# Performance work log

Hardware: AMD Instinct MI355X
Metric: run time of the kernel (lower is better)

## Reference

```python
import jax, jax.numpy as jnp
import numpy as np

B, T, D, H = 4, 2048, 1024, 16
HD = D // H  # 64
NEG = -np.finfo(np.float32).max


def setup_inputs() -> dict:
    key = jax.random.key(0)
    ks = jax.random.split(key, 9)
    s = 1.0 / np.sqrt(D)
    return {
        "x": jax.random.normal(ks[0], (B, T, D), jnp.float32),
        "wq": jax.random.normal(ks[1], (D, D), jnp.float32) * s,
        "bq": jax.random.normal(ks[2], (D,), jnp.float32) * 0.02,
        "wk": jax.random.normal(ks[3], (D, D), jnp.float32) * s,
        "bk": jax.random.normal(ks[4], (D,), jnp.float32) * 0.02,
        "wv": jax.random.normal(ks[5], (D, D), jnp.float32) * s,
        "bv": jax.random.normal(ks[6], (D,), jnp.float32) * 0.02,
        "wo": jax.random.normal(ks[7], (D, D), jnp.float32) * s,
        "bo": jax.random.normal(ks[8], (D,), jnp.float32) * 0.02,
    }


def reference(x, wq, bq, wk, bk, wv, bv, wo, bo):
    b, t, d = x.shape
    # separate Q, K, V projections, reshape to (B, H, T, HD)
    def proj(w, bias):
        y = x @ w + bias
        return y.reshape(b, t, H, HD).transpose(0, 2, 1, 3)
    q = proj(wq, bq)
    k = proj(wk, bk)
    v = proj(wv, bv)
    scale = 1.0 / np.sqrt(HD).astype(np.float32)
    scores = jnp.einsum("bhqd,bhkd->bhqk", q, k) * scale  # (B,H,T,T)
    # causal mask: -max_float on strictly upper triangle (matches source)
    mask = jnp.triu(jnp.full((t, t), NEG, jnp.float32), k=1)
    attn = jax.nn.softmax(scores + mask, axis=-1)
    out = jnp.einsum("bhqk,bhkd->bhqd", attn, v)
    out = out.transpose(0, 2, 1, 3).reshape(b, t, d)
    return out @ wo + bo
```

## Files before the change

kernel.cpp:

```cpp
#include <hip/hip_runtime.h>

typedef __bf16 bf16x8 __attribute__((ext_vector_type(8)));
typedef float f32x4 __attribute__((ext_vector_type(4)));

#define B_ 4
#define T_ 2048
#define D_ 1024
#define H_ 16
#define HD_ 64
#define M_ 8192
#define QSCALE 0.1803368801111204f

__device__ __forceinline__ ushort f2b(float f) {
  union { float f; unsigned u; } v; v.f = f;
  unsigned u = v.u;
  return (ushort)((u + 0x7FFFu + ((u >> 16) & 1u)) >> 16);
}

__device__ __forceinline__ unsigned pkbf(float a, float b) {
  union { float f; unsigned u; } va, vb; va.f = a; vb.f = b;
  return __builtin_amdgcn_perm(vb.u + 0x8000u, va.u + 0x8000u, 0x07060302u);
}

__device__ __forceinline__ void gll16(const void* g, void* l) {
  __builtin_amdgcn_global_load_lds(
      (const __attribute__((address_space(1))) unsigned*)g,
      (__attribute__((address_space(3))) unsigned*)l, 16, 0, 0);
}

__global__ __launch_bounds__(256) void cast_x_kernel(const float* __restrict__ x,
                                                     ushort* __restrict__ xb) {
  int idx = blockIdx.x * 256 + threadIdx.x;
  float4 v = ((const float4*)x)[idx];
  ushort4 o;
  o.x = f2b(v.x); o.y = f2b(v.y); o.z = f2b(v.z); o.w = f2b(v.w);
  ((ushort4*)xb)[idx] = o;
}

__global__ __launch_bounds__(256) void transpose_w_kernel(
    const float* __restrict__ wq, const float* __restrict__ wk,
    const float* __restrict__ wv, const float* __restrict__ wo,
    ushort* __restrict__ wt_qkv, ushort* __restrict__ wt_o) {
  __shared__ float tile[32][33];
  int z = blockIdx.z;
  const float* src = (z == 0) ? wq : (z == 1) ? wk : (z == 2) ? wv : wo;
  ushort* dst = (z < 3) ? (wt_qkv + (size_t)z * D_ * D_) : wt_o;
  int n0 = blockIdx.x * 32, k0 = blockIdx.y * 32;
  int tx = threadIdx.x & 31, ty = threadIdx.x >> 5;
  for (int i = 0; i < 4; i++) {
    int r = ty + i * 8;
    tile[r][tx] = src[(size_t)(k0 + r) * D_ + n0 + tx];
  }
  __syncthreads();
  for (int i = 0; i < 4; i++) {
    int r = ty + i * 8;
    dst[(size_t)(n0 + r) * D_ + k0 + tx] = f2b(tile[tx][r]);
  }
}

__global__ __launch_bounds__(256) void gemm_kernel(
    const ushort* __restrict__ A, const ushort* __restrict__ Bt, int mode,
    const float* __restrict__ bias_q, const float* __restrict__ bias_k,
    const float* __restrict__ bias_v,
    ushort* __restrict__ qb, ushort* __restrict__ kb, ushort* __restrict__ vtb,
    float* __restrict__ outf) {
  __shared__ ushort As[2][128][64];
  __shared__ ushort Bs[2][128][64];
  int tid = threadIdx.x;
  int wave = tid >> 6, lane = tid & 63, lrow = lane >> 4, lcol = lane & 15;

  int gx = gridDim.x;
  int nwg = gx * gridDim.y;
  int orig = blockIdx.x + gx * blockIdx.y;
  int work = (orig & 7) * (nwg >> 3) + (orig >> 3);
  int m0 = (work / gx) * 128, n0 = (work % gx) * 128;
  int wm = (wave & 1) * 64, wn = (wave >> 1) * 64;

  int rb = tid >> 3;
  int dc = tid & 7;
  int scv = dc ^ (rb & 7);
  const ushort* aBase = A + (size_t)(m0 + rb) * D_ + scv * 8;
  const ushort* bBase = Bt + (size_t)(n0 + rb) * D_ + scv * 8;

  f32x4 zero = {0.f, 0.f, 0.f, 0.f};
  f32x4 acc[4][4];
  for (int i = 0; i < 4; i++)
    for (int j = 0; j < 4; j++) acc[i][j] = zero;

  int swz = lcol & 7;

  auto stage = [&](int buf, int k) {
#pragma unroll
    for (int g = 0; g < 4; g++) {
      gll16(aBase + (size_t)(32 * g) * D_ + k, &As[buf][0][0] + tid * 8 + g * 2048);
      gll16(bBase + (size_t)(32 * g) * D_ + k, &Bs[buf][0][0] + tid * 8 + g * 2048);
    }
  };

  stage(0, 0);

  for (int k0 = 0; k0 < D_; k0 += 64) {
    int cur = (k0 >> 6) & 1, nxt = cur ^ 1;
    __syncthreads();
    if (k0 + 64 < D_) stage(nxt, k0 + 64);

    for (int ks = 0; ks < 2; ks++) {
      bf16x8 af[4], bf[4];
      int ch = ((ks * 4 + lrow) ^ swz) * 8;
      for (int mt = 0; mt < 4; mt++)
        af[mt] = *(const bf16x8*)&As[cur][wm + mt * 16 + lcol][ch];
      for (int nt = 0; nt < 4; nt++)
        bf[nt] = *(const bf16x8*)&Bs[cur][wn + nt * 16 + lcol][ch];
      for (int mt = 0; mt < 4; mt++)
        for (int nt = 0; nt < 4; nt++)
          acc[mt][nt] = __builtin_amdgcn_mfma_f32_16x16x32_bf16(
              af[mt], bf[nt], acc[mt][nt], 0, 0, 0);
    }
  }

  if (mode == 0) {
    int proj = n0 >> 10;
    const float* bias = (proj == 0) ? bias_q : (proj == 1) ? bias_k : bias_v;
    for (int mt = 0; mt < 4; mt++) {
      int gm0 = m0 + wm + mt * 16 + lrow * 4;
      int b = gm0 >> 11, tp = gm0 & 2047;
      for (int nt = 0; nt < 4; nt++) {
        int gn = n0 + wn + nt * 16 + lcol;
        int inner = gn & 1023;
        int h = inner >> 6, hd = inner & 63;
        float bv = bias[inner];
        if (proj == 0) {
          size_t base = ((size_t)(b * H_ + h) * T_ + tp) * HD_ + hd;
          for (int r = 0; r < 4; r++)
            qb[base + (size_t)r * HD_] = f2b((acc[mt][nt][r] + bv) * QSCALE);
        } else if (proj == 1) {
          size_t base = ((size_t)(b * H_ + h) * T_ + tp) * HD_ + hd;
          for (int r = 0; r < 4; r++)
            kb[base + (size_t)r * HD_] = f2b(acc[mt][nt][r] + bv);
        } else {
          ushort4 pk;
          pk.x = f2b(acc[mt][nt][0] + bv);
          pk.y = f2b(acc[mt][nt][1] + bv);
          pk.z = f2b(acc[mt][nt][2] + bv);
          pk.w = f2b(acc[mt][nt][3] + bv);
          *(ushort4*)&vtb[((size_t)(b * H_ + h) * HD_ + hd) * T_ + tp] = pk;
        }
      }
    }
  } else {
    for (int mt = 0; mt < 4; mt++) {
      int gm0 = m0 + wm + mt * 16 + lrow * 4;
      for (int nt = 0; nt < 4; nt++) {
        int gn = n0 + wn + nt * 16 + lcol;
        float bv = bias_q[gn];
        for (int r = 0; r < 4; r++)
          outf[(size_t)(gm0 + r) * D_ + gn] = acc[mt][nt][r] + bv;
      }
    }
  }
}

__global__ __launch_bounds__(256) void flash_kernel(
    const ushort* __restrict__ qb, const ushort* __restrict__ kb,
    const ushort* __restrict__ vtb, ushort* __restrict__ ob) {
  __shared__ ushort Ks2[2][64][64];
  __shared__ ushort Vs2[2][64][64];
  __shared__ ushort Ps[4][32][64];
  int tid = threadIdx.x;
  int wave = tid >> 6, lane = tid & 63, lrow = lane >> 4, lcol = lane & 15;

  int bid = blockIdx.x + (blockIdx.y << 3);
  int xcd = bid & 7;
  int slot = bid >> 3;
  int bh = xcd * 8 + (slot >> 3);
  int p = slot & 7;
  int qb0 = 15 - p, qb1 = p;
  int b = bh >> 4, h = bh & 15;
  const ushort* qp = qb + (size_t)bh * T_ * HD_;
  const ushort* kh = kb + (size_t)bh * T_ * HD_;
  const ushort* vh = vtb + (size_t)bh * HD_ * T_;

  int n0 = 2 * qb0 + 2;
  int ntot = n0 + 2 * qb1 + 2;

  int r0 = tid >> 3, dc = tid & 7;
  int wsl = (dc ^ (r0 & 7)) * 8;
  int rsw = lcol & 7;

  uint4 kr0, kr1, vr0, vr1;
  auto gload = [&](int jt) {
    kr0 = *(const uint4*)&kh[(size_t)(jt * 64 + r0) * HD_ + dc * 8];
    kr1 = *(const uint4*)&kh[(size_t)(jt * 64 + r0 + 32) * HD_ + dc * 8];
    vr0 = *(const uint4*)&vh[(size_t)r0 * T_ + jt * 64 + dc * 8];
    vr1 = *(const uint4*)&vh[(size_t)(r0 + 32) * T_ + jt * 64 + dc * 8];
  };
  auto swrite = [&](int buf) {
    *(uint4*)&Ks2[buf][r0][wsl] = kr0;
    *(uint4*)&Ks2[buf][r0 + 32][wsl] = kr1;
    *(uint4*)&Vs2[buf][r0][wsl] = vr0;
    *(uint4*)&Vs2[buf][r0 + 32][wsl] = vr1;
  };

  bf16x8 af1;
  {
    __bf16 ov = (__bf16)((lcol == 0) ? 1.0f : 0.0f);
    for (int i2 = 0; i2 < 8; i2++) af1[i2] = ov;
  }

  f32x4 zero = {0.f, 0.f, 0.f, 0.f};

  gload(0);
  swrite(0);
  gload(1);
  __syncthreads();

  int q0wA = qb0 * 128 + wave * 32, q0wB = qb1 * 128 + wave * 32;
  bf16x8 qfA[2][2], qfB[2][2];
#pragma unroll
  for (int qh = 0; qh < 2; qh++)
#pragma unroll
    for (int ks = 0; ks < 2; ks++) {
      qfA[qh][ks] = *(const bf16x8*)&qp[(size_t)(q0wA + qh * 16 + lcol) * HD_ +
                                        ks * 32 + lrow * 8];
      qfB[qh][ks] = *(const bf16x8*)&qp[(size_t)(q0wB + qh * 16 + lcol) * HD_ +
                                        ks * 32 + lrow * 8];
    }

  auto run_pass = [&](int qblk, int q0w, int base, const bf16x8 qf[2][2]) {
    f32x4 accO[2][4];
    f32x4 accS[2];
#pragma unroll
    for (int qh = 0; qh < 2; qh++) {
      accS[qh] = zero;
      for (int mt = 0; mt < 4; mt++) accO[qh][mt] = zero;
    }

    int nj = 2 * qblk + 2;
    for (int j = 0; j < nj; j++) {
      int g = base + j, cur = g & 1;
      bool active = (j * 64 <= q0w + 31);

      if (active) {
        f32x4 st[2][4];
#pragma unroll
        for (int qh = 0; qh < 2; qh++)
          for (int mt = 0; mt < 4; mt++) st[qh][mt] = zero;
        __builtin_amdgcn_s_setprio(1);
#pragma unroll
        for (int ks = 0; ks < 2; ks++)
#pragma unroll
          for (int mt = 0; mt < 4; mt++) {
            bf16x8 kf = *(const bf16x8*)&Ks2[cur][mt * 16 + lcol]
                                            [((ks * 4 + lrow) ^ rsw) * 8];
            st[0][mt] = __builtin_amdgcn_mfma_f32_16x16x32_bf16(kf, qf[0][ks], st[0][mt], 0, 0, 0);
            st[1][mt] = __builtin_amdgcn_mfma_f32_16x16x32_bf16(kf, qf[1][ks], st[1][mt], 0, 0, 0);
          }
        __builtin_amdgcn_s_setprio(0);

        if (j >= 2 * qblk) {
#pragma unroll
          for (int qh = 0; qh < 2; qh++) {
            int q_g = q0w + qh * 16 + lcol;
#pragma unroll
            for (int mt = 0; mt < 4; mt++)
              for (int r = 0; r < 4; r++) {
                int kv_g = j * 64 + mt * 16 + lrow * 4 + r;
                if (kv_g > q_g) st[qh][mt][r] = -1e30f;
              }
          }
        }

#pragma unroll
        for (int qh = 0; qh < 2; qh++)
          for (int mt = 0; mt < 4; mt++)
            for (int r = 0; r < 4; r++)
              st[qh][mt][r] = __builtin_amdgcn_exp2f(st[qh][mt][r]);

#pragma unroll
        for (int qh = 0; qh < 2; qh++)
          for (int mt = 0; mt < 4; mt++) {
            uint2 pk;
            pk.x = pkbf(st[qh][mt][0], st[qh][mt][1]);
            pk.y = pkbf(st[qh][mt][2], st[qh][mt][3]);
            int sl = ((2 * mt + (lrow >> 1)) ^ rsw) * 8 + (lrow & 1) * 4;
            *(uint2*)&Ps[wave][qh * 16 + lcol][sl] = pk;
          }

        __builtin_amdgcn_s_setprio(1);
#pragma unroll
        for (int ks = 0; ks < 2; ks++) {
          int ch = ((ks * 4 + lrow) ^ rsw) * 8;
          bf16x8 pf0 = *(const bf16x8*)&Ps[wave][lcol][ch];
          bf16x8 pf1 = *(const bf16x8*)&Ps[wave][16 + lcol][ch];
          accS[0] = __builtin_amdgcn_mfma_f32_16x16x32_bf16(af1, pf0, accS[0], 0, 0, 0);
          accS[1] = __builtin_amdgcn_mfma_f32_16x16x32_bf16(af1, pf1, accS[1], 0, 0, 0);
#pragma unroll
          for (int mt = 0; mt < 4; mt++) {
            bf16x8 vf = *(const bf16x8*)&Vs2[cur][mt * 16 + lcol][ch];
            accO[0][mt] = __builtin_amdgcn_mfma_f32_16x16x32_bf16(vf, pf0, accO[0][mt], 0, 0, 0);
            accO[1][mt] = __builtin_amdgcn_mfma_f32_16x16x32_bf16(vf, pf1, accO[1][mt], 0, 0, 0);
          }
        }
        __builtin_amdgcn_s_setprio(0);
      }

      if (g + 1 < ntot) swrite(cur ^ 1);
      if (g + 2 < ntot) {
        int s = g + 2;
        gload(s < n0 ? s : s - n0);
      }
      __syncthreads();
    }

#pragma unroll
    for (int qh = 0; qh < 2; qh++) {
      float lsum = __shfl(accS[qh][0], lcol);
      float linv = 1.f / lsum;
      int t = q0w + qh * 16 + lcol;
      size_t base2 = ((size_t)b * T_ + t) * D_ + h * HD_;
#pragma unroll
      for (int mt = 0; mt < 4; mt++) {
        uint2 pk;
        pk.x = pkbf(accO[qh][mt][0] * linv, accO[qh][mt][1] * linv);
        pk.y = pkbf(accO[qh][mt][2] * linv, accO[qh][mt][3] * linv);
        *(uint2*)&ob[base2 + mt * 16 + lrow * 4] = pk;
      }
    }
  };

  run_pass(qb0, q0wA, 0, qfA);
  run_pass(qb1, q0wB, n0, qfB);
}

extern "C" void kernel_launch(void* const* d_in, const int* in_sizes, int n_in,
                              void* d_out, int out_size, void* d_ws, size_t ws_size,
                              hipStream_t stream) {
  (void)in_sizes; (void)n_in; (void)out_size; (void)ws_size;
  const float* x  = (const float*)d_in[0];
  const float* wq = (const float*)d_in[1];
  const float* bq = (const float*)d_in[2];
  const float* wk = (const float*)d_in[3];
  const float* bk = (const float*)d_in[4];
  const float* wv = (const float*)d_in[5];
  const float* bv = (const float*)d_in[6];
  const float* wo = (const float*)d_in[7];
  const float* bo = (const float*)d_in[8];
  float* out = (float*)d_out;

  char* ws = (char*)d_ws;
  ushort* xb     = (ushort*)(ws);
  ushort* wt_qkv = (ushort*)(ws + 16777216);
  ushort* wt_o   = (ushort*)(ws + 23068672);
  ushort* qb     = (ushort*)(ws + 25165824);
  ushort* kb     = (ushort*)(ws + 41943040);
  ushort* vtb    = (ushort*)(ws + 58720256);
  ushort* ob     = (ushort*)(ws + 75497472);

  cast_x_kernel<<<8192, 256, 0, stream>>>(x, xb);
  transpose_w_kernel<<<dim3(32, 32, 4), 256, 0, stream>>>(wq, wk, wv, wo, wt_qkv, wt_o);
  gemm_kernel<<<dim3(24, 64), 256, 0, stream>>>(xb, wt_qkv, 0, bq, bk, bv, qb, kb, vtb, nullptr);
  flash_kernel<<<dim3(8, 64), 256, 0, stream>>>(qb, kb, vtb, ob);
  gemm_kernel<<<dim3(8, 64), 256, 0, stream>>>(ob, wt_o, 1, bo, nullptr, nullptr,
                                               nullptr, nullptr, nullptr, out);
}
```

Before: 247.0 us.

## Share K/V tiles between paired query blocks and vectorize Q/K epilogue stores

The flash kernel now processes both paired query blocks (15-p and p) in one loop over key/value tiles. Each K/V tile staged in LDS feeds both blocks, instead of the kernel making two sequential passes that reload the smaller block's tiles. This needs two sets of output accumulators in registers, which may raise register pressure and lower occupancy. It also remaps block-to-head assignment with a phase that alternates pairing order. Separately, the Q/K projection epilogue uses lane shuffles and byte permutes to assemble four contiguous bf16 values per lane, replacing scattered 2-byte stores with 8-byte stores.

```diff
diff --git a/kernel.cpp b/kernel.cpp
--- a/kernel.cpp
+++ b/kernel.cpp
@@ -121,23 +121,46 @@
   if (mode == 0) {
     int proj = n0 >> 10;
     const float* bias = (proj == 0) ? bias_q : (proj == 1) ? bias_k : bias_v;
-    for (int mt = 0; mt < 4; mt++) {
-      int gm0 = m0 + wm + mt * 16 + lrow * 4;
-      int b = gm0 >> 11, tp = gm0 & 2047;
-      for (int nt = 0; nt < 4; nt++) {
-        int gn = n0 + wn + nt * 16 + lcol;
-        int inner = gn & 1023;
-        int h = inner >> 6, hd = inner & 63;
-        float bv = bias[inner];
-        if (proj == 0) {
-          size_t base = ((size_t)(b * H_ + h) * T_ + tp) * HD_ + hd;
-          for (int r = 0; r < 4; r++)
-            qb[base + (size_t)r * HD_] = f2b((acc[mt][nt][r] + bv) * QSCALE);
-        } else if (proj == 1) {
-          size_t base = ((size_t)(b * H_ + h) * T_ + tp) * HD_ + hd;
-          for (int r = 0; r < 4; r++)
-            kb[base + (size_t)r * HD_] = f2b(acc[mt][nt][r] + bv);
-        } else {
+    if (proj < 2) {
+      ushort* dst = (proj == 0) ? qb : kb;
+      bool isq = (proj == 0);
+      int c0 = lcol & 1, c1 = lcol & 2;
+      for (int mt = 0; mt < 4; mt++) {
+        int gm0 = m0 + wm + mt * 16 + lrow * 4;
+        int t = gm0 + (lcol & 3);
+        int b = t >> 11, tp = t & 2047;
+        for (int nt = 0; nt < 4; nt++) {
+          int gn = n0 + wn + nt * 16 + lcol;
+          int inner = gn & 1023;
+          float bv = bias[inner];
+          float v0 = acc[mt][nt][0] + bv, v1 = acc[mt][nt][1] + bv;
+          float v2 = acc[mt][nt][2] + bv, v3 = acc[mt][nt][3] + bv;
+          if (isq) { v0 *= QSCALE; v1 *= QSCALE; v2 *= QSCALE; v3 *= QSCALE; }
+          unsigned p0 = ((unsigned)f2b(v1) << 16) | f2b(v0);
+          unsigned p1 = ((unsigned)f2b(v3) << 16) | f2b(v2);
+          unsigned x0 = __shfl_xor(p0, 1), x1 = __shfl_xor(p1, 1);
+          unsigned a0 = c0 ? __builtin_amdgcn_perm(p0, x0, 0x07060302u)
+                           : __builtin_amdgcn_perm(x0, p0, 0x05040100u);
+          unsigned a1 = c0 ? __builtin_amdgcn_perm(p1, x1, 0x07060302u)
+                           : __builtin_amdgcn_perm(x1, p1, 0x05040100u);
+          unsigned y0 = __shfl_xor(a0, 2), y1 = __shfl_xor(a1, 2);
+          uint2 q2;
+          q2.x = c1 ? y1 : a0;
+          q2.y = c1 ? a1 : y0;
+          int innerb = (n0 + wn + nt * 16 + (lcol & ~3)) & 1023;
+          int h = innerb >> 6, hd0 = innerb & 63;
+          *(uint2*)&dst[((size_t)(b * H_ + h) * T_ + tp) * HD_ + hd0] = q2;
+        }
+      }
+    } else {
+      for (int mt = 0; mt < 4; mt++) {
+        int gm0 = m0 + wm + mt * 16 + lrow * 4;
+        int b = gm0 >> 11, tp = gm0 & 2047;
+        for (int nt = 0; nt < 4; nt++) {
+          int gn = n0 + wn + nt * 16 + lcol;
+          int inner = gn & 1023;
+          int h = inner >> 6, hd = inner & 63;
+          float bv = bias[inner];
           ushort4 pk;
           pk.x = f2b(acc[mt][nt][0] + bv);
           pk.y = f2b(acc[mt][nt][1] + bv);
@@ -160,6 +183,72 @@
   }
 }
 
+#define QCOMP(qblk_, q0w_, qfv, accOv, accSv)                                   \
+  do {                                                                          \
+    f32x4 st[2][4];                                                             \
+    for (int qh = 0; qh < 2; qh++)                                              \
+      for (int mt = 0; mt < 4; mt++) st[qh][mt] = zero;                         \
+    __builtin_amdgcn_s_setprio(1);                                              \
+    _Pragma("unroll")                                                           \
+    for (int ks = 0; ks < 2; ks++)                                              \
+      _Pragma("unroll")                                                         \
+      for (int mt = 0; mt < 4; mt++) {                                          \
+        bf16x8 kf = *(const bf16x8*)&Ks2[cur][mt * 16 + lcol]                   \
+                                        [((ks * 4 + lrow) ^ rsw) * 8];          \
+        st[0][mt] = __builtin_amdgcn_mfma_f32_16x16x32_bf16(kf, qfv[0][ks],     \
+                                                            st[0][mt], 0, 0, 0);\
+        st[1][mt] = __builtin_amdgcn_mfma_f32_16x16x32_bf16(kf, qfv[1][ks],     \
+                                                            st[1][mt], 0, 0, 0);\
+      }                                                                         \
+    __builtin_amdgcn_s_setprio(0);                                              \
+    if (j >= 2 * (qblk_)) {                                                     \
+      _Pragma("unroll")                                                         \
+      for (int qh = 0; qh < 2; qh++) {                                          \
+        int q_g = (q0w_) + qh * 16 + lcol;                                      \
+        _Pragma("unroll")                                                       \
+        for (int mt = 0; mt < 4; mt++)                                          \
+          for (int r = 0; r < 4; r++) {                                         \
+            int kv_g = j * 64 + mt * 16 + lrow * 4 + r;                         \
+            if (kv_g > q_g) st[qh][mt][r] = -1e30f;                             \
+          }                                                                     \
+      }                                                                         \
+    }                                                                           \
+    _Pragma("unroll")                                                           \
+    for (int qh = 0; qh < 2; qh++)                                              \
+      for (int mt = 0; mt < 4; mt++)                                            \
+        for (int r = 0; r < 4; r++)                                             \
+          st[qh][mt][r] = __builtin_amdgcn_exp2f(st[qh][mt][r]);                \
+    _Pragma("unroll")                                                           \
+    for (int qh = 0; qh < 2; qh++)                                              \
+      for (int mt = 0; mt < 4; mt++) {                                          \
+        uint2 pk;                                                               \
+        pk.x = pkbf(st[qh][mt][0], st[qh][mt][1]);                              \
+        pk.y = pkbf(st[qh][mt][2], st[qh][mt][3]);                              \
+        int sl = ((2 * mt + (lrow >> 1)) ^ rsw) * 8 + (lrow & 1) * 4;           \
+        *(uint2*)&Ps[wave][qh * 16 + lcol][sl] = pk;                            \
+      }                                                                         \
+    __builtin_amdgcn_s_setprio(1);                                              \
+    _Pragma("unroll")                                                           \
+    for (int ks = 0; ks < 2; ks++) {                                            \
+      int ch = ((ks * 4 + lrow) ^ rsw) * 8;                                     \
+      bf16x8 pf0 = *(const bf16x8*)&Ps[wave][lcol][ch];                         \
+      bf16x8 pf1 = *(const bf16x8*)&Ps[wave][16 + lcol][ch];                    \
+      accSv[0] = __builtin_amdgcn_mfma_f32_16x16x32_bf16(af1, pf0, accSv[0],    \
+                                                         0, 0, 0);              \
+      accSv[1] = __builtin_amdgcn_mfma_f32_16x16x32_bf16(af1, pf1, accSv[1],    \
+                                                         0, 0, 0);              \
+      _Pragma("unroll")                                                         \
+      for (int mt = 0; mt < 4; mt++) {                                          \
+        bf16x8 vf = *(const bf16x8*)&Vs2[cur][mt * 16 + lcol][ch];              \
+        accOv[0][mt] = __builtin_amdgcn_mfma_f32_16x16x32_bf16(vf, pf0,         \
+                                                    accOv[0][mt], 0, 0, 0);     \
+        accOv[1][mt] = __builtin_amdgcn_mfma_f32_16x16x32_bf16(vf, pf1,         \
+                                                    accOv[1][mt], 0, 0, 0);     \
+      }                                                                         \
+    }                                                                           \
+    __builtin_amdgcn_s_setprio(0);                                              \
+  } while (0)
+
 __global__ __launch_bounds__(256) void flash_kernel(
     const ushort* __restrict__ qb, const ushort* __restrict__ kb,
     const ushort* __restrict__ vtb, ushort* __restrict__ ob) {
@@ -172,16 +261,18 @@
   int bid = blockIdx.x + (blockIdx.y << 3);
   int xcd = bid & 7;
   int slot = bid >> 3;
-  int bh = xcd * 8 + (slot >> 3);
-  int p = slot & 7;
-  int qb0 = 15 - p, qb1 = p;
+  int phase = slot >> 5;
+  int j5 = slot & 31;
+  int pm = j5 & 7;
+  int bh = xcd * 8 + (j5 >> 3) + phase * 4;
+  int p = phase ? 7 - pm : pm;
+  int qbA = 15 - p, qbB = p;
   int b = bh >> 4, h = bh & 15;
   const ushort* qp = qb + (size_t)bh * T_ * HD_;
   const ushort* kh = kb + (size_t)bh * T_ * HD_;
   const ushort* vh = vtb + (size_t)bh * HD_ * T_;
 
-  int n0 = 2 * qb0 + 2;
-  int ntot = n0 + 2 * qb1 + 2;
+  int njA = 2 * qbA + 2, njB = 2 * qbB + 2;
 
   int r0 = tid >> 3, dc = tid & 7;
   int wsl = (dc ^ (r0 & 7)) * 8;
@@ -214,7 +305,7 @@
   gload(1);
   __syncthreads();
 
-  int q0wA = qb0 * 128 + wave * 32, q0wB = qb1 * 128 + wave * 32;
+  int q0wA = qbA * 128 + wave * 32, q0wB = qbB * 128 + wave * 32;
   bf16x8 qfA[2][2], qfB[2][2];
 #pragma unroll
   for (int qh = 0; qh < 2; qh++)
@@ -226,110 +317,52 @@
                                         ks * 32 + lrow * 8];
     }
 
-  auto run_pass = [&](int qblk, int q0w, int base, const bf16x8 qf[2][2]) {
-    f32x4 accO[2][4];
-    f32x4 accS[2];
-#pragma unroll
-    for (int qh = 0; qh < 2; qh++) {
-      accS[qh] = zero;
-      for (int mt = 0; mt < 4; mt++) accO[qh][mt] = zero;
-    }
-
-    int nj = 2 * qblk + 2;
-    for (int j = 0; j < nj; j++) {
-      int g = base + j, cur = g & 1;
-      bool active = (j * 64 <= q0w + 31);
-
-      if (active) {
-        f32x4 st[2][4];
-#pragma unroll
-        for (int qh = 0; qh < 2; qh++)
-          for (int mt = 0; mt < 4; mt++) st[qh][mt] = zero;
-        __builtin_amdgcn_s_setprio(1);
-#pragma unroll
-        for (int ks = 0; ks < 2; ks++)
-#pragma unroll
-          for (int mt = 0; mt < 4; mt++) {
-            bf16x8 kf = *(const bf16x8*)&Ks2[cur][mt * 16 + lcol]
-                                            [((ks * 4 + lrow) ^ rsw) * 8];
-            st[0][mt] = __builtin_amdgcn_mfma_f32_16x16x32_bf16(kf, qf[0][ks], st[0][mt], 0, 0, 0);
-            st[1][mt] = __builtin_amdgcn_mfma_f32_16x16x32_bf16(kf, qf[1][ks], st[1][mt], 0, 0, 0);
-          }
-        __builtin_amdgcn_s_setprio(0);
-
-        if (j >= 2 * qblk) {
-#pragma unroll
-          for (int qh = 0; qh < 2; qh++) {
-            int q_g = q0w + qh * 16 + lcol;
-#pragma unroll
-            for (int mt = 0; mt < 4; mt++)
-              for (int r = 0; r < 4; r++) {
-                int kv_g = j * 64 + mt * 16 + lrow * 4 + r;
-                if (kv_g > q_g) st[qh][mt][r] = -1e30f;
-              }
-          }
-        }
-
-#pragma unroll
-        for (int qh = 0; qh < 2; qh++)
-          for (int mt = 0; mt < 4; mt++)
-            for (int r = 0; r < 4; r++)
-              st[qh][mt][r] = __builtin_amdgcn_exp2f(st[qh][mt][r]);
-
-#pragma unroll
-        for (int qh = 0; qh < 2; qh++)
-          for (int mt = 0; mt < 4; mt++) {
-            uint2 pk;
-            pk.x = pkbf(st[qh][mt][0], st[qh][mt][1]);
-            pk.y = pkbf(st[qh][mt][2], st[qh][mt][3]);
-            int sl = ((2 * mt + (lrow >> 1)) ^ rsw) * 8 + (lrow & 1) * 4;
-            *(uint2*)&Ps[wave][qh * 16 + lcol][sl] = pk;
-          }
-
-        __builtin_amdgcn_s_setprio(1);
-#pragma unroll
-        for (int ks = 0; ks < 2; ks++) {
-          int ch = ((ks * 4 + lrow) ^ rsw) * 8;
-          bf16x8 pf0 = *(const bf16x8*)&Ps[wave][lcol][ch];
-          bf16x8 pf1 = *(const bf16x8*)&Ps[wave][16 + lcol][ch];
-          accS[0] = __builtin_amdgcn_mfma_f32_16x16x32_bf16(af1, pf0, accS[0], 0, 0, 0);
-          accS[1] = __builtin_amdgcn_mfma_f32_16x16x32_bf16(af1, pf1, accS[1], 0, 0, 0);
-#pragma unroll
-          for (int mt = 0; mt < 4; mt++) {
-            bf16x8 vf = *(const bf16x8*)&Vs2[cur][mt * 16 + lcol][ch];
-            accO[0][mt] = __builtin_amdgcn_mfma_f32_16x16x32_bf16(vf, pf0, accO[0][mt], 0, 0, 0);
-            accO[1][mt] = __builtin_amdgcn_mfma_f32_16x16x32_bf16(vf, pf1, accO[1][mt], 0, 0, 0);
-          }
-        }
-        __builtin_amdgcn_s_setprio(0);
-      }
-
-      if (g + 1 < ntot) swrite(cur ^ 1);
-      if (g + 2 < ntot) {
-        int s = g + 2;
-        gload(s < n0 ? s : s - n0);
-      }
-      __syncthreads();
-    }
-
-#pragma unroll
-    for (int qh = 0; qh < 2; qh++) {
-      float lsum = __shfl(accS[qh][0], lcol);
-      float linv = 1.f / lsum;
-      int t = q0w + qh * 16 + lcol;
-      size_t base2 = ((size_t)b * T_ + t) * D_ + h * HD_;
-#pragma unroll
-      for (int mt = 0; mt < 4; mt++) {
-        uint2 pk;
-        pk.x = pkbf(accO[qh][mt][0] * linv, accO[qh][mt][1] * linv);
-        pk.y = pkbf(accO[qh][mt][2] * linv, accO[qh][mt][3] * linv);
-        *(uint2*)&ob[base2 + mt * 16 + lrow * 4] = pk;
-      }
-    }
-  };
-
-  run_pass(qb0, q0wA, 0, qfA);
-  run_pass(qb1, q0wB, n0, qfB);
+  f32x4 accOA[2][4], accOB[2][4];
+  f32x4 accSA[2], accSB[2];
+#pragma unroll
+  for (int qh = 0; qh < 2; qh++) {
+    accSA[qh] = zero; accSB[qh] = zero;
+    for (int mt = 0; mt < 4; mt++) { accOA[qh][mt] = zero; accOB[qh][mt] = zero; }
+  }
+
+  for (int j = 0; j < njA; j++) {
+    int cur = j & 1;
+    if (j * 64 <= q0wA + 31) QCOMP(qbA, q0wA, qfA, accOA, accSA);
+    if (j * 64 <= q0wB + 31) QCOMP(qbB, q0wB, qfB, accOB, accSB);
+    if (j + 1 < njA) swrite(cur ^ 1);
+    if (j + 2 < njA) gload(j + 2);
+    __syncthreads();
+  }
+  (void)njB;
+
+#pragma unroll
+  for (int qh = 0; qh < 2; qh++) {
+    float lsum = __shfl(accSA[qh][0], lcol);
+    float linv = 1.f / lsum;
+    int t = q0wA + qh * 16 + lcol;
+    size_t base2 = ((size_t)b * T_ + t) * D_ + h * HD_;
+#pragma unroll
+    for (int mt = 0; mt < 4; mt++) {
+      uint2 pk;
+      pk.x = pkbf(accOA[qh][mt][0] * linv, accOA[qh][mt][1] * linv);
+      pk.y = pkbf(accOA[qh][mt][2] * linv, accOA[qh][mt][3] * linv);
+      *(uint2*)&ob[base2 + mt * 16 + lrow * 4] = pk;
+    }
+  }
+#pragma unroll
+  for (int qh = 0; qh < 2; qh++) {
+    float lsum = __shfl(accSB[qh][0], lcol);
+    float linv = 1.f / lsum;
+    int t = q0wB + qh * 16 + lcol;
+    size_t base2 = ((size_t)b * T_ + t) * D_ + h * HD_;
+#pragma unroll
+    for (int mt = 0; mt < 4; mt++) {
+      uint2 pk;
+      pk.x = pkbf(accOB[qh][mt][0] * linv, accOB[qh][mt][1] * linv);
+      pk.y = pkbf(accOB[qh][mt][2] * linv, accOB[qh][mt][3] * linv);
+      *(uint2*)&ob[base2 + mt * 16 + lrow * 4] = pk;
+    }
+  }
 }
 
 extern "C" void kernel_launch(void* const* d_in, const int* in_sizes, int n_in,
```

Measured after the change: 246.8 us. No clear change (-0.0%).
